# Kernel optimization log

Hardware: AMD Instinct MI355X
Metric: run time of the kernel (lower is better)

The kernel has to match this reference:

```python
import jax, jax.numpy as jnp
import numpy as np

NUM_LAYER = 5
EMB = 300
BN_EPS = 1e-5
NUM_BOND_TYPE = 6
NUM_BOND_DIR = 3
SELF_LOOP_TYPE = 4  # pretrain-gnns self-loop edge attr = [4, 0]


def setup_inputs() -> dict:
    key = jax.random.key(0)
    ks = jax.random.split(key, 12)
    N, E, D = 100000, 250000, EMB
    x = jax.random.normal(ks[0], (N, D), dtype=jnp.float32)
    edge_index = jax.random.randint(ks[1], (2, E), 0, N, dtype=jnp.int64)
    edge_attr = jax.random.randint(ks[2], (E, 2), 0, 3, dtype=jnp.int64)
    L = NUM_LAYER
    W1 = jax.random.normal(ks[3], (L, D, 2 * D), dtype=jnp.float32) * 0.05
    b1 = jnp.zeros((L, 2 * D), dtype=jnp.float32)
    W2 = jax.random.normal(ks[4], (L, 2 * D, D), dtype=jnp.float32) * 0.05
    b2 = jnp.zeros((L, D), dtype=jnp.float32)
    E1 = jax.random.normal(ks[5], (L, NUM_BOND_TYPE, D), dtype=jnp.float32) * 0.05
    E2 = jax.random.normal(ks[6], (L, NUM_BOND_DIR, D), dtype=jnp.float32) * 0.05
    gamma = jnp.ones((L, D), dtype=jnp.float32)
    beta = jnp.zeros((L, D), dtype=jnp.float32)
    return {"x": x, "edge_index": edge_index, "edge_attr": edge_attr,
            "W1": W1, "b1": b1, "W2": W2, "b2": b2,
            "E1": E1, "E2": E2, "gamma": gamma, "beta": beta}


def reference(x, edge_index, edge_attr, W1, b1, W2, b2, E1, E2, gamma, beta):
    N = x.shape[0]
    src, dst = edge_index[0], edge_index[1]
    bt, bd = edge_attr[:, 0], edge_attr[:, 1]
    h = x
    for l in range(NUM_LAYER):
        # GINEConv: message = x_j + edge_embedding, aggr='add', with self loops
        edge_emb = E1[l][bt] + E2[l][bd]                 # [E, D]
        self_emb = E1[l][SELF_LOOP_TYPE] + E2[l][0]      # [D]
        msg = h[src] + edge_emb                          # [E, D] gather
        agg = jax.ops.segment_sum(msg, dst, num_segments=N) + h + self_emb
        # update MLP: Linear(D,2D) -> ReLU -> Linear(2D,D)
        m = jax.nn.relu(agg @ W1[l] + b1[l]) @ W2[l] + b2[l]
        # BatchNorm1d in training mode (batch stats over nodes, biased var)
        mu = m.mean(axis=0)
        var = m.var(axis=0)
        m = (m - mu) * jax.lax.rsqrt(var + BN_EPS) * gamma[l] + beta[l]
        if l < NUM_LAYER - 1:  # ReLU on all but last layer; dropout ratio 0 -> no-op
            m = jax.nn.relu(m)
        h = m
    return h  # JK == 'last'
```

## Files before the change

kernel.cpp:

```cpp
#include <hip/hip_runtime.h>
#include <hip/hip_bf16.h>

#define NN 100000
#define NE 250000
#define DD 300
#define DDB 304
#define NL 5
#define MPAD 100096
#define KA1 320
#define N1 608
#define N1T 640
#define K2 608
#define N2T 384
#define NBLK 391
#define NCMB 19

typedef __attribute__((ext_vector_type(8))) short short8;
typedef __attribute__((ext_vector_type(4))) float f32x4;

#define GLBP(x) ((const __attribute__((address_space(1))) unsigned int*)(x))
#define LDSP(x) ((__attribute__((address_space(3))) unsigned int*)(x))
#define WAITV(N) asm volatile("s_waitcnt vmcnt(" #N ")" ::: "memory")

__device__ __forceinline__ ushort f2bf(float f){
  unsigned u = __float_as_uint(f);
  u += 0x7FFFu + ((u >> 16) & 1u);
  return (ushort)(u >> 16);
}
__device__ __forceinline__ float bf2f(ushort h){
  return __uint_as_float((unsigned)h << 16);
}
__device__ __forceinline__ unsigned pk2(float a, float b){
  return (unsigned)f2bf(a) | ((unsigned)f2bf(b) << 16);
}

__global__ void prep_weights(const float* __restrict__ W1, const float* __restrict__ W2,
                             ushort* __restrict__ W1T, ushort* __restrict__ W2T){
  int idx = blockIdx.x * 256 + threadIdx.x;
  const int total1 = NL * N1T * KA1;
  const int total2 = NL * N2T * K2;
  if (idx < total1){
    int l = idx / (N1T * KA1);
    int rem = idx % (N1T * KA1);
    int n = rem / KA1, k = rem % KA1;
    float v = (n < 2*DD && k < DD) ? W1[(size_t)l*DD*2*DD + (size_t)k*2*DD + n] : 0.0f;
    W1T[idx] = f2bf(v);
  } else {
    int idx2 = idx - total1;
    if (idx2 < total2){
      int l = idx2 / (N2T * K2);
      int rem = idx2 % (N2T * K2);
      int n = rem / K2, k = rem % K2;
      float v = (n < DD && k < 2*DD) ? W2[(size_t)l*2*DD*DD + (size_t)k*DD + n] : 0.0f;
      W2T[idx2] = f2bf(v);
    }
  }
}

__global__ void prep_ctab(const float* __restrict__ E1, const float* __restrict__ E2,
                          float* __restrict__ ctab){
  int idx = blockIdx.x * 256 + threadIdx.x;
  if (idx >= NL * NCMB * DDB) return;
  int l = idx / (NCMB * DDB);
  int rem = idx % (NCMB * DDB);
  int c = rem / DDB, d = rem % DDB;
  float v = 0.0f;
  if (d < DD){
    int bt = (c < 18) ? (c / 3) : 4;
    int bd = (c < 18) ? (c % 3) : 0;
    v = E1[(size_t)l*6*DD + bt*DD + d] + E2[(size_t)l*3*DD + bd*DD + d];
  }
  ctab[idx] = v;
}

__global__ void csr_count(const int* __restrict__ ei, int* __restrict__ deg){
  int e = blockIdx.x * 256 + threadIdx.x;
  if (e < NE) atomicAdd(&deg[ei[NE + e]], 1);
}

__global__ void scan_blk(const int* __restrict__ deg, int* __restrict__ rs, int* __restrict__ bsum){
  __shared__ int tmp[256];
  int i = blockIdx.x * 256 + threadIdx.x;
  int v = (i < NN) ? deg[i] : 0;
  tmp[threadIdx.x] = v;
  __syncthreads();
  #pragma unroll
  for (int off = 1; off < 256; off <<= 1){
    int t = (threadIdx.x >= off) ? tmp[threadIdx.x - off] : 0;
    __syncthreads();
    tmp[threadIdx.x] += t;
    __syncthreads();
  }
  if (i < NN) rs[i] = tmp[threadIdx.x] - v;
  if (threadIdx.x == 255) bsum[blockIdx.x] = tmp[255];
}

__global__ void scan_top(int* __restrict__ bsum){
  __shared__ int tmp[512];
  int v = (threadIdx.x < NBLK) ? bsum[threadIdx.x] : 0;
  tmp[threadIdx.x] = v;
  __syncthreads();
  #pragma unroll
  for (int off = 1; off < 512; off <<= 1){
    int t = (threadIdx.x >= off) ? tmp[threadIdx.x - off] : 0;
    __syncthreads();
    tmp[threadIdx.x] += t;
    __syncthreads();
  }
  if (threadIdx.x < NBLK) bsum[threadIdx.x] = tmp[threadIdx.x] - v;
}

__global__ void scan_add(int* __restrict__ rs, const int* __restrict__ bsum){
  int i = blockIdx.x * 256 + threadIdx.x;
  if (i < NN) rs[i] += bsum[blockIdx.x];
  if (i == 0) rs[NN] = NE;
}

__global__ void csr_fill(const int* __restrict__ ei, const int* __restrict__ ea,
                         const int* __restrict__ rs, int* __restrict__ cursor,
                         int* __restrict__ edges){
  int e = blockIdx.x * 256 + threadIdx.x;
  if (e < NE){
    int dst = ei[NE + e];
    int src = ei[e];
    int c = ea[2*e] * 3 + ea[2*e + 1];
    int p = rs[dst] + atomicAdd(&cursor[dst], 1);
    edges[p] = src | (c << 20);
  }
}

template<int HBF>
__global__ __launch_bounds__(256) void gather_agg(
    const void* __restrict__ hp, const float2* __restrict__ ss,
    const float* __restrict__ ctab_l,
    const int* __restrict__ rs, const int* __restrict__ edges,
    ushort* __restrict__ agg)
{
  int lane = threadIdx.x & 63;
  int wq = __builtin_amdgcn_readfirstlane(threadIdx.x >> 6);
  int wid = blockIdx.x * 4 + wq;
  int nw = gridDim.x * 4;
  int dA = lane * 4;
  int dB = 256 + lane * 4;
  bool laneB  = (lane < 16);
  bool validB = (dB + 3 < DD + 3) && (dB < DD);

  float scA[4], shA[4], scB[4], shB[4];
  if (HBF){
    #pragma unroll
    for (int j = 0; j < 4; ++j){
      float2 s = ss[dA + j]; scA[j] = s.x; shA[j] = s.y;
    }
    if (validB){
      #pragma unroll
      for (int j = 0; j < 4; ++j){
        float2 s = ss[dB + j]; scB[j] = s.x; shB[j] = s.y;
      }
    }
  }

  const float*  hf = (const float*)hp;
  const ushort* hb = (const ushort*)hp;
  const float* ctS = ctab_l + 18*DDB;

  for (int row = wid; row < MPAD; row += nw){
    float a0=0,a1=0,a2=0,a3=0, b0=0,b1=0,b2=0,b3=0;
    if (row < NN){
      {
        if (HBF){
          uint2 hw = *(const uint2*)(hb + (size_t)row*DDB + dA);
          float h0=bf2f((ushort)hw.x), h1=bf2f((ushort)(hw.x>>16));
          float h2=bf2f((ushort)hw.y), h3=bf2f((ushort)(hw.y>>16));
          a0 = fmaxf(h0*scA[0]+shA[0],0.f) + ctS[dA+0];
          a1 = fmaxf(h1*scA[1]+shA[1],0.f) + ctS[dA+1];
          a2 = fmaxf(h2*scA[2]+shA[2],0.f) + ctS[dA+2];
          a3 = fmaxf(h3*scA[3]+shA[3],0.f) + ctS[dA+3];
          if (validB){
            uint2 hv = *(const uint2*)(hb + (size_t)row*DDB + dB);
            b0 = fmaxf(bf2f((ushort)hv.x)*scB[0]+shB[0],0.f)      + ctS[dB+0];
            b1 = fmaxf(bf2f((ushort)(hv.x>>16))*scB[1]+shB[1],0.f)+ ctS[dB+1];
            b2 = fmaxf(bf2f((ushort)hv.y)*scB[2]+shB[2],0.f)      + ctS[dB+2];
            b3 = fmaxf(bf2f((ushort)(hv.y>>16))*scB[3]+shB[3],0.f)+ ctS[dB+3];
          }
        } else {
          float4 hv = *(const float4*)(hf + (size_t)row*DD + dA);
          a0 = hv.x + ctS[dA+0]; a1 = hv.y + ctS[dA+1];
          a2 = hv.z + ctS[dA+2]; a3 = hv.w + ctS[dA+3];
          if (validB){
            float4 hv2 = *(const float4*)(hf + (size_t)row*DD + dB);
            b0 = hv2.x + ctS[dB+0]; b1 = hv2.y + ctS[dB+1];
            b2 = hv2.z + ctS[dB+2]; b3 = hv2.w + ctS[dB+3];
          }
        }
      }
      int p = rs[row], pe = rs[row + 1];
      for (; p < pe; ++p){
        int ew = edges[p];
        int src = ew & 0xFFFFF;
        const float* ct = ctab_l + (ew >> 20)*DDB;
        if (HBF){
          uint2 hw = *(const uint2*)(hb + (size_t)src*DDB + dA);
          float h0=bf2f((ushort)hw.x), h1=bf2f((ushort)(hw.x>>16));
          float h2=bf2f((ushort)hw.y), h3=bf2f((ushort)(hw.y>>16));
          a0 += fmaxf(h0*scA[0]+shA[0],0.f) + ct[dA+0];
          a1 += fmaxf(h1*scA[1]+shA[1],0.f) + ct[dA+1];
          a2 += fmaxf(h2*scA[2]+shA[2],0.f) + ct[dA+2];
          a3 += fmaxf(h3*scA[3]+shA[3],0.f) + ct[dA+3];
          if (validB){
            uint2 hv = *(const uint2*)(hb + (size_t)src*DDB + dB);
            b0 += fmaxf(bf2f((ushort)hv.x)*scB[0]+shB[0],0.f)      + ct[dB+0];
            b1 += fmaxf(bf2f((ushort)(hv.x>>16))*scB[1]+shB[1],0.f)+ ct[dB+1];
            b2 += fmaxf(bf2f((ushort)hv.y)*scB[2]+shB[2],0.f)      + ct[dB+2];
            b3 += fmaxf(bf2f((ushort)(hv.y>>16))*scB[3]+shB[3],0.f)+ ct[dB+3];
          }
        } else {
          float4 hv = *(const float4*)(hf + (size_t)src*DD + dA);
          a0 += hv.x + ct[dA+0]; a1 += hv.y + ct[dA+1];
          a2 += hv.z + ct[dA+2]; a3 += hv.w + ct[dA+3];
          if (validB){
            float4 hv2 = *(const float4*)(hf + (size_t)src*DD + dB);
            b0 += hv2.x + ct[dB+0]; b1 += hv2.y + ct[dB+1];
            b2 += hv2.z + ct[dB+2]; b3 += hv2.w + ct[dB+3];
          }
        }
      }
    }
    ushort* ag = agg + (size_t)row*KA1;
    uint2 oA; oA.x = pk2(a0, a1); oA.y = pk2(a2, a3);
    *(uint2*)(ag + dA) = oA;
    if (laneB){
      uint2 oB;
      if (validB){ oB.x = pk2(b0, b1); oB.y = pk2(b2, b3); }
      else       { oB.x = 0; oB.y = 0; }
      *(uint2*)(ag + dB) = oB;
    }
  }
}

template<int OUT_BF16, int RELU, int STATS>
__global__ __launch_bounds__(512) void gemm_lds(
    const ushort* __restrict__ A, int lda,
    const ushort* __restrict__ B, int ldb,
    void* __restrict__ Cp, int ldc,
    int kTiles, const float* __restrict__ bias, int biasN,
    int Mvalid, int Nvalid, int nColTiles, float* __restrict__ statf)
{
  __shared__ ushort As[3][8192];
  __shared__ ushort Bs[3][4096];
  int tid = threadIdx.x;
  int lane = tid & 63, w = tid >> 6;
  int wm = (w >> 1) * 64, wn = (w & 1) * 64;

  int nwg = gridDim.x;
  int q = nwg >> 3, r = nwg & 7;
  int xcd = blockIdx.x & 7, idx = blockIdx.x >> 3;
  int bid = (xcd < r ? xcd * (q + 1) : r * (q + 1) + (xcd - r) * q) + idx;
  int m0 = (bid / nColTiles) * 256;
  int n0 = (bid % nColTiles) * 128;

  int r0 = tid >> 2;
  int kc = ((tid & 3) ^ ((tid >> 3) & 3)) * 8;
  const ushort* Ap = A + (size_t)(m0 + r0)*lda + kc;
  const ushort* Bp = B + (size_t)(n0 + r0)*ldb + kc;

  f32x4 acc[4][4] = {};

#define STAGE(buf, kt) do { \
    int _ko = (kt) * 32; \
    __builtin_amdgcn_global_load_lds(GLBP(Ap + _ko),                   LDSP(&As[buf][w*512]),        16, 0, 0); \
    __builtin_amdgcn_global_load_lds(GLBP(Ap + _ko + (size_t)128*lda), LDSP(&As[buf][w*512 + 4096]), 16, 0, 0); \
    __builtin_amdgcn_global_load_lds(GLBP(Bp + _ko),                   LDSP(&Bs[buf][w*512]),        16, 0, 0); \
  } while (0)

  STAGE(0, 0);
  STAGE(1, 1);
  WAITV(3);
  __builtin_amdgcn_s_barrier();

  int fr = lane & 15;
  int ko8 = (((lane >> 4) ^ ((fr >> 1) & 3))) * 8;
  int cur = 0;
  for (int kt = 0; kt < kTiles; ++kt){
    int sb = cur + 2; if (sb >= 3) sb -= 3;
    if (kt + 2 < kTiles) STAGE(sb, kt + 2);
    short8 af[4], bfv[4];
    #pragma unroll
    for (int i = 0; i < 4; ++i)
      af[i] = *(const short8*)&As[cur][(wm + i*16 + fr)*32 + ko8];
    #pragma unroll
    for (int j = 0; j < 4; ++j)
      bfv[j] = *(const short8*)&Bs[cur][(wn + j*16 + fr)*32 + ko8];
    #pragma unroll
    for (int i = 0; i < 4; ++i)
      #pragma unroll
      for (int j = 0; j < 4; ++j)
        acc[i][j] = __builtin_amdgcn_mfma_f32_16x16x32_bf16(af[i], bfv[j], acc[i][j], 0, 0, 0);
    if (kt + 1 < kTiles){
      if (kt + 2 < kTiles) WAITV(3);
      else                 WAITV(0);
      __builtin_amdgcn_s_barrier();
    }
    cur = cur + 1; if (cur >= 3) cur = 0;
  }
#undef STAGE

  int cc = lane & 15, cr = (lane >> 4) * 4;
  float ps[4], pq[4];
  if (STATS){
    #pragma unroll
    for (int j = 0; j < 4; ++j){ ps[j] = 0.0f; pq[j] = 0.0f; }
  }
  #pragma unroll
  for (int i = 0; i < 4; ++i){
    #pragma unroll
    for (int j = 0; j < 4; ++j){
      int col = n0 + wn + j*16 + cc;
      if (col >= Nvalid) continue;
      float bv = (col < biasN) ? bias[col] : 0.0f;
      #pragma unroll
      for (int r2 = 0; r2 < 4; ++r2){
        int row = m0 + wm + i*16 + cr + r2;
        if (row < Mvalid){
          float v = acc[i][j][r2] + bv;
          if (RELU) v = fmaxf(v, 0.0f);
          if (OUT_BF16) ((ushort*)Cp)[(size_t)row*ldc + col] = f2bf(v);
          else          ((float*) Cp)[(size_t)row*ldc + col] = v;
          if (STATS){ ps[j] += v; pq[j] += v * v; }
        }
      }
    }
  }
  if (STATS){
    #pragma unroll
    for (int j = 0; j < 4; ++j){
      float s = ps[j], qv = pq[j];
      s += __shfl_xor(s, 16); qv += __shfl_xor(qv, 16);
      s += __shfl_xor(s, 32); qv += __shfl_xor(qv, 32);
      int col = n0 + wn + j*16 + cc;
      if ((lane >> 4) == 0 && col < Nvalid){
        unsafeAtomicAdd(&statf[col], s);
        unsafeAtomicAdd(&statf[N2T + col], qv);
      }
    }
  }
}

__global__ void make_norm(const float* __restrict__ statf, const float* __restrict__ gamma,
                          const float* __restrict__ beta, float2* __restrict__ ss){
  int d = threadIdx.x;
  if (d >= DD) return;
  double mu = (double)statf[d] / (double)NN;
  double var = (double)statf[N2T + d] / (double)NN - mu * mu;
  float inv = rsqrtf((float)var + 1e-5f);
  float sc = inv * gamma[d];
  ss[d] = make_float2(sc, beta[d] - (float)mu * sc);
}

__global__ void apply_norm(const float* __restrict__ m2, const float2* __restrict__ ss,
                           float* __restrict__ out){
  int row = blockIdx.x;
  int d = threadIdx.x;
  if (d >= DD) return;
  float2 s = ss[d];
  out[(size_t)row*DD + d] = m2[(size_t)row*DD + d] * s.x + s.y;
}

extern "C" void kernel_launch(void* const* d_in, const int* in_sizes, int n_in,
                              void* d_out, int out_size, void* d_ws, size_t ws_size,
                              hipStream_t stream) {
  const float* x     = (const float*)d_in[0];
  const int*   ei    = (const int*)  d_in[1];
  const int*   ea    = (const int*)  d_in[2];
  const float* W1    = (const float*)d_in[3];
  const float* b1    = (const float*)d_in[4];
  const float* W2    = (const float*)d_in[5];
  const float* b2    = (const float*)d_in[6];
  const float* E1    = (const float*)d_in[7];
  const float* E2    = (const float*)d_in[8];
  const float* gamma = (const float*)d_in[9];
  const float* beta  = (const float*)d_in[10];

  char* p = (char*)d_ws;
  float*  m2buf = (float*) p; p += (size_t)NN * DD * 4;
  ushort* m2bf  = (ushort*)p; p += (size_t)NN * DDB * 2;
  ushort* agg   = (ushort*)p; p += (size_t)MPAD * KA1 * 2;
  ushort* m1    = (ushort*)p; p += (size_t)MPAD * N1 * 2;
  ushort* W1T   = (ushort*)p; p += (size_t)NL * N1T * KA1 * 2;
  ushort* W2T   = (ushort*)p; p += (size_t)NL * N2T * K2 * 2;
  float*  ctab  = (float*) p; p += (size_t)NL * NCMB * DDB * 4;
  int*    deg   = (int*)   p; p += (size_t)NN * 4;
  int*    rs    = (int*)   p; p += (size_t)(NN + 16) * 4;
  int*    bsum  = (int*)   p; p += (size_t)512 * 4;
  int*    cursor= (int*)   p; p += (size_t)NN * 4;
  int*    edges = (int*)   p; p += (size_t)NE * 4;
  float*  statf = (float*) p; p += (size_t)2 * N2T * 4;
  float2* ss    = (float2*)p;

  {
    int total = NL*N1T*KA1 + NL*N2T*K2;
    prep_weights<<<(total + 255)/256, 256, 0, stream>>>(W1, W2, W1T, W2T);
    int tc = NL * NCMB * DDB;
    prep_ctab<<<(tc + 255)/256, 256, 0, stream>>>(E1, E2, ctab);
  }
  hipMemsetAsync(deg, 0, (size_t)NN*4, stream);
  hipMemsetAsync(cursor, 0, (size_t)NN*4, stream);
  csr_count<<<(NE + 255)/256, 256, 0, stream>>>(ei, deg);
  scan_blk<<<NBLK, 256, 0, stream>>>(deg, rs, bsum);
  scan_top<<<1, 512, 0, stream>>>(bsum);
  scan_add<<<NBLK, 256, 0, stream>>>(rs, bsum);
  csr_fill<<<(NE + 255)/256, 256, 0, stream>>>(ei, ea, rs, cursor, edges);

  for (int l = 0; l < NL; ++l){
    const float* ctab_l = ctab + (size_t)l * NCMB * DDB;

    if (l == 0)
      gather_agg<0><<<1024, 256, 0, stream>>>(x, nullptr, ctab_l, rs, edges, agg);
    else
      gather_agg<1><<<1024, 256, 0, stream>>>(m2bf, ss, ctab_l, rs, edges, agg);

    gemm_lds<1,1,0><<<(MPAD/256) * (N1T/128), 512, 0, stream>>>(
        agg, KA1, W1T + (size_t)l*N1T*KA1, KA1, m1, N1, KA1/32,
        b1 + (size_t)l*2*DD, 2*DD, MPAD, N1, N1T/128, nullptr);

    hipMemsetAsync(statf, 0, (size_t)2*N2T*4, stream);

    if (l < NL - 1)
      gemm_lds<1,0,1><<<(MPAD/256) * (N2T/128), 512, 0, stream>>>(
          m1, N1, W2T + (size_t)l*N2T*K2, K2, m2bf, DDB, K2/32,
          b2 + (size_t)l*DD, DD, NN, DD, N2T/128, statf);
    else
      gemm_lds<0,0,1><<<(MPAD/256) * (N2T/128), 512, 0, stream>>>(
          m1, N1, W2T + (size_t)l*N2T*K2, K2, m2buf, DD, K2/32,
          b2 + (size_t)l*DD, DD, NN, DD, N2T/128, statf);

    make_norm<<<1, 320, 0, stream>>>(statf, gamma + (size_t)l*DD, beta + (size_t)l*DD, ss);
  }
  apply_norm<<<NN, 320, 0, stream>>>(m2buf, ss, (float*)d_out);
}
```

Before: 1.529 ms.

## Shrink GEMM tile to 128x128 with 256 threads and 5-stage LDS pipeline

The GEMM workgroup drops from 512 threads on a 256x128 tile to 256 threads on a 128x128 tile. The LDS pipeline grows from 3 to 5 buffers with a prefetch distance of 4 and matching vmcnt waits. The aim is more workgroups, better occupancy and deeper latency hiding for the short K loops (10 and 19 tiles). The cost is less A-tile reuse per workgroup and more B traffic, plus a cosmetic cleanup of the gather kernel.

```diff
diff --git a/kernel.cpp b/kernel.cpp
--- a/kernel.cpp
+++ b/kernel.cpp
@@ -143,7 +143,7 @@
   int dA = lane * 4;
   int dB = 256 + lane * 4;
   bool laneB  = (lane < 16);
-  bool validB = (dB + 3 < DD + 3) && (dB < DD);
+  bool validB = (dB < DD);
 
   float scA[4], shA[4], scB[4], shB[4];
   if (HBF){
@@ -166,31 +166,27 @@
   for (int row = wid; row < MPAD; row += nw){
     float a0=0,a1=0,a2=0,a3=0, b0=0,b1=0,b2=0,b3=0;
     if (row < NN){
-      {
-        if (HBF){
-          uint2 hw = *(const uint2*)(hb + (size_t)row*DDB + dA);
-          float h0=bf2f((ushort)hw.x), h1=bf2f((ushort)(hw.x>>16));
-          float h2=bf2f((ushort)hw.y), h3=bf2f((ushort)(hw.y>>16));
-          a0 = fmaxf(h0*scA[0]+shA[0],0.f) + ctS[dA+0];
-          a1 = fmaxf(h1*scA[1]+shA[1],0.f) + ctS[dA+1];
-          a2 = fmaxf(h2*scA[2]+shA[2],0.f) + ctS[dA+2];
-          a3 = fmaxf(h3*scA[3]+shA[3],0.f) + ctS[dA+3];
-          if (validB){
-            uint2 hv = *(const uint2*)(hb + (size_t)row*DDB + dB);
-            b0 = fmaxf(bf2f((ushort)hv.x)*scB[0]+shB[0],0.f)      + ctS[dB+0];
-            b1 = fmaxf(bf2f((ushort)(hv.x>>16))*scB[1]+shB[1],0.f)+ ctS[dB+1];
-            b2 = fmaxf(bf2f((ushort)hv.y)*scB[2]+shB[2],0.f)      + ctS[dB+2];
-            b3 = fmaxf(bf2f((ushort)(hv.y>>16))*scB[3]+shB[3],0.f)+ ctS[dB+3];
-          }
-        } else {
-          float4 hv = *(const float4*)(hf + (size_t)row*DD + dA);
-          a0 = hv.x + ctS[dA+0]; a1 = hv.y + ctS[dA+1];
-          a2 = hv.z + ctS[dA+2]; a3 = hv.w + ctS[dA+3];
-          if (validB){
-            float4 hv2 = *(const float4*)(hf + (size_t)row*DD + dB);
-            b0 = hv2.x + ctS[dB+0]; b1 = hv2.y + ctS[dB+1];
-            b2 = hv2.z + ctS[dB+2]; b3 = hv2.w + ctS[dB+3];
-          }
+      if (HBF){
+        uint2 hw = *(const uint2*)(hb + (size_t)row*DDB + dA);
+        a0 = fmaxf(bf2f((ushort)hw.x)*scA[0]+shA[0],0.f)      + ctS[dA+0];
+        a1 = fmaxf(bf2f((ushort)(hw.x>>16))*scA[1]+shA[1],0.f)+ ctS[dA+1];
+        a2 = fmaxf(bf2f((ushort)hw.y)*scA[2]+shA[2],0.f)      + ctS[dA+2];
+        a3 = fmaxf(bf2f((ushort)(hw.y>>16))*scA[3]+shA[3],0.f)+ ctS[dA+3];
+        if (validB){
+          uint2 hv = *(const uint2*)(hb + (size_t)row*DDB + dB);
+          b0 = fmaxf(bf2f((ushort)hv.x)*scB[0]+shB[0],0.f)      + ctS[dB+0];
+          b1 = fmaxf(bf2f((ushort)(hv.x>>16))*scB[1]+shB[1],0.f)+ ctS[dB+1];
+          b2 = fmaxf(bf2f((ushort)hv.y)*scB[2]+shB[2],0.f)      + ctS[dB+2];
+          b3 = fmaxf(bf2f((ushort)(hv.y>>16))*scB[3]+shB[3],0.f)+ ctS[dB+3];
+        }
+      } else {
+        float4 hv = *(const float4*)(hf + (size_t)row*DD + dA);
+        a0 = hv.x + ctS[dA+0]; a1 = hv.y + ctS[dA+1];
+        a2 = hv.z + ctS[dA+2]; a3 = hv.w + ctS[dA+3];
+        if (validB){
+          float4 hv2 = *(const float4*)(hf + (size_t)row*DD + dB);
+          b0 = hv2.x + ctS[dB+0]; b1 = hv2.y + ctS[dB+1];
+          b2 = hv2.z + ctS[dB+2]; b3 = hv2.w + ctS[dB+3];
         }
       }
       int p = rs[row], pe = rs[row + 1];
@@ -200,12 +196,10 @@
         const float* ct = ctab_l + (ew >> 20)*DDB;
         if (HBF){
           uint2 hw = *(const uint2*)(hb + (size_t)src*DDB + dA);
-          float h0=bf2f((ushort)hw.x), h1=bf2f((ushort)(hw.x>>16));
-          float h2=bf2f((ushort)hw.y), h3=bf2f((ushort)(hw.y>>16));
-          a0 += fmaxf(h0*scA[0]+shA[0],0.f) + ct[dA+0];
-          a1 += fmaxf(h1*scA[1]+shA[1],0.f) + ct[dA+1];
-          a2 += fmaxf(h2*scA[2]+shA[2],0.f) + ct[dA+2];
-          a3 += fmaxf(h3*scA[3]+shA[3],0.f) + ct[dA+3];
+          a0 += fmaxf(bf2f((ushort)hw.x)*scA[0]+shA[0],0.f)      + ct[dA+0];
+          a1 += fmaxf(bf2f((ushort)(hw.x>>16))*scA[1]+shA[1],0.f)+ ct[dA+1];
+          a2 += fmaxf(bf2f((ushort)hw.y)*scA[2]+shA[2],0.f)      + ct[dA+2];
+          a3 += fmaxf(bf2f((ushort)(hw.y>>16))*scA[3]+shA[3],0.f)+ ct[dA+3];
           if (validB){
             uint2 hv = *(const uint2*)(hb + (size_t)src*DDB + dB);
             b0 += fmaxf(bf2f((ushort)hv.x)*scB[0]+shB[0],0.f)      + ct[dB+0];
@@ -238,15 +232,15 @@
 }
 
 template<int OUT_BF16, int RELU, int STATS>
-__global__ __launch_bounds__(512) void gemm_lds(
+__global__ __launch_bounds__(256) void gemm_lds(
     const ushort* __restrict__ A, int lda,
     const ushort* __restrict__ B, int ldb,
     void* __restrict__ Cp, int ldc,
     int kTiles, const float* __restrict__ bias, int biasN,
     int Mvalid, int Nvalid, int nColTiles, float* __restrict__ statf)
 {
-  __shared__ ushort As[3][8192];
-  __shared__ ushort Bs[3][4096];
+  __shared__ ushort As[5][4096];
+  __shared__ ushort Bs[5][4096];
   int tid = threadIdx.x;
   int lane = tid & 63, w = tid >> 6;
   int wm = (w >> 1) * 64, wn = (w & 1) * 64;
@@ -255,7 +249,7 @@
   int q = nwg >> 3, r = nwg & 7;
   int xcd = blockIdx.x & 7, idx = blockIdx.x >> 3;
   int bid = (xcd < r ? xcd * (q + 1) : r * (q + 1) + (xcd - r) * q) + idx;
-  int m0 = (bid / nColTiles) * 256;
+  int m0 = (bid / nColTiles) * 128;
   int n0 = (bid % nColTiles) * 128;
 
   int r0 = tid >> 2;
@@ -267,22 +261,22 @@
 
 #define STAGE(buf, kt) do { \
     int _ko = (kt) * 32; \
-    __builtin_amdgcn_global_load_lds(GLBP(Ap + _ko),                   LDSP(&As[buf][w*512]),        16, 0, 0); \
-    __builtin_amdgcn_global_load_lds(GLBP(Ap + _ko + (size_t)128*lda), LDSP(&As[buf][w*512 + 4096]), 16, 0, 0); \
-    __builtin_amdgcn_global_load_lds(GLBP(Bp + _ko),                   LDSP(&Bs[buf][w*512]),        16, 0, 0); \
+    __builtin_amdgcn_global_load_lds(GLBP(Ap + _ko),                  LDSP(&As[buf][w*512]),        16, 0, 0); \
+    __builtin_amdgcn_global_load_lds(GLBP(Ap + _ko + (size_t)64*lda), LDSP(&As[buf][w*512 + 2048]), 16, 0, 0); \
+    __builtin_amdgcn_global_load_lds(GLBP(Bp + _ko),                  LDSP(&Bs[buf][w*512]),        16, 0, 0); \
+    __builtin_amdgcn_global_load_lds(GLBP(Bp + _ko + (size_t)64*ldb), LDSP(&Bs[buf][w*512 + 2048]), 16, 0, 0); \
   } while (0)
 
-  STAGE(0, 0);
-  STAGE(1, 1);
-  WAITV(3);
+  STAGE(0, 0); STAGE(1, 1); STAGE(2, 2); STAGE(3, 3);
+  WAITV(12);
   __builtin_amdgcn_s_barrier();
 
   int fr = lane & 15;
   int ko8 = (((lane >> 4) ^ ((fr >> 1) & 3))) * 8;
   int cur = 0;
   for (int kt = 0; kt < kTiles; ++kt){
-    int sb = cur + 2; if (sb >= 3) sb -= 3;
-    if (kt + 2 < kTiles) STAGE(sb, kt + 2);
+    int sb = cur + 4; if (sb >= 5) sb -= 5;
+    if (kt + 4 < kTiles) STAGE(sb, kt + 4);
     short8 af[4], bfv[4];
     #pragma unroll
     for (int i = 0; i < 4; ++i)
@@ -296,11 +290,14 @@
       for (int j = 0; j < 4; ++j)
         acc[i][j] = __builtin_amdgcn_mfma_f32_16x16x32_bf16(af[i], bfv[j], acc[i][j], 0, 0, 0);
     if (kt + 1 < kTiles){
-      if (kt + 2 < kTiles) WAITV(3);
-      else                 WAITV(0);
+      int rem = kTiles - kt;
+      if      (rem >= 5) WAITV(12);
+      else if (rem == 4) WAITV(8);
+      else if (rem == 3) WAITV(4);
+      else               WAITV(0);
       __builtin_amdgcn_s_barrier();
     }
-    cur = cur + 1; if (cur >= 3) cur = 0;
+    cur = cur + 1; if (cur >= 5) cur = 0;
   }
 #undef STAGE
 
@@ -418,18 +415,18 @@
     else
       gather_agg<1><<<1024, 256, 0, stream>>>(m2bf, ss, ctab_l, rs, edges, agg);
 
-    gemm_lds<1,1,0><<<(MPAD/256) * (N1T/128), 512, 0, stream>>>(
+    gemm_lds<1,1,0><<<(MPAD/128) * (N1T/128), 256, 0, stream>>>(
         agg, KA1, W1T + (size_t)l*N1T*KA1, KA1, m1, N1, KA1/32,
         b1 + (size_t)l*2*DD, 2*DD, MPAD, N1, N1T/128, nullptr);
 
     hipMemsetAsync(statf, 0, (size_t)2*N2T*4, stream);
 
     if (l < NL - 1)
-      gemm_lds<1,0,1><<<(MPAD/256) * (N2T/128), 512, 0, stream>>>(
+      gemm_lds<1,0,1><<<(MPAD/128) * (N2T/128), 256, 0, stream>>>(
           m1, N1, W2T + (size_t)l*N2T*K2, K2, m2bf, DDB, K2/32,
           b2 + (size_t)l*DD, DD, NN, DD, N2T/128, statf);
     else
-      gemm_lds<0,0,1><<<(MPAD/256) * (N2T/128), 512, 0, stream>>>(
+      gemm_lds<0,0,1><<<(MPAD/128) * (N2T/128), 256, 0, stream>>>(
           m1, N1, W2T + (size_t)l*N2T*K2, K2, m2buf, DD, K2/32,
           b2 + (size_t)l*DD, DD, NN, DD, N2T/128, statf);
 
```

Result: slower. 1.888 ms (+23.5%).

## Add persistent first-layer GEMM keeping a weight column tile resident in LDS

Applied to the files above, without the earlier changes.

Replaces the generic tiled GEMM for the first MLP linear with a persistent kernel. Each workgroup loads one 128-column slice of W1 into LDS once, then streams 3-4 row tiles of the aggregated features through a triple-buffered async global-to-LDS pipeline. Bias and ReLU are applied in registers, and the output is staged through LDS so it can be written with coalesced 16-byte stores. This is meant to cut repeated weight loads and per-tile launch overhead, at the cost of much more LDS per block and lower occupancy. The gather kernel gets only cosmetic cleanups.

```diff
diff --git a/kernel.cpp b/kernel.cpp
--- a/kernel.cpp
+++ b/kernel.cpp
@@ -143,7 +143,7 @@
   int dA = lane * 4;
   int dB = 256 + lane * 4;
   bool laneB  = (lane < 16);
-  bool validB = (dB + 3 < DD + 3) && (dB < DD);
+  bool validB = (dB < DD);
 
   float scA[4], shA[4], scB[4], shB[4];
   if (HBF){
@@ -164,33 +164,29 @@
   const float* ctS = ctab_l + 18*DDB;
 
   for (int row = wid; row < MPAD; row += nw){
-    float a0=0,a1=0,a2=0,a3=0, b0=0,b1=0,b2=0,b3=0;
+    float a0=0,a1=0,a2=0,a3=0, b0=0,b1v=0,b2v=0,b3=0;
     if (row < NN){
-      {
-        if (HBF){
-          uint2 hw = *(const uint2*)(hb + (size_t)row*DDB + dA);
-          float h0=bf2f((ushort)hw.x), h1=bf2f((ushort)(hw.x>>16));
-          float h2=bf2f((ushort)hw.y), h3=bf2f((ushort)(hw.y>>16));
-          a0 = fmaxf(h0*scA[0]+shA[0],0.f) + ctS[dA+0];
-          a1 = fmaxf(h1*scA[1]+shA[1],0.f) + ctS[dA+1];
-          a2 = fmaxf(h2*scA[2]+shA[2],0.f) + ctS[dA+2];
-          a3 = fmaxf(h3*scA[3]+shA[3],0.f) + ctS[dA+3];
-          if (validB){
-            uint2 hv = *(const uint2*)(hb + (size_t)row*DDB + dB);
-            b0 = fmaxf(bf2f((ushort)hv.x)*scB[0]+shB[0],0.f)      + ctS[dB+0];
-            b1 = fmaxf(bf2f((ushort)(hv.x>>16))*scB[1]+shB[1],0.f)+ ctS[dB+1];
-            b2 = fmaxf(bf2f((ushort)hv.y)*scB[2]+shB[2],0.f)      + ctS[dB+2];
-            b3 = fmaxf(bf2f((ushort)(hv.y>>16))*scB[3]+shB[3],0.f)+ ctS[dB+3];
-          }
-        } else {
-          float4 hv = *(const float4*)(hf + (size_t)row*DD + dA);
-          a0 = hv.x + ctS[dA+0]; a1 = hv.y + ctS[dA+1];
-          a2 = hv.z + ctS[dA+2]; a3 = hv.w + ctS[dA+3];
-          if (validB){
-            float4 hv2 = *(const float4*)(hf + (size_t)row*DD + dB);
-            b0 = hv2.x + ctS[dB+0]; b1 = hv2.y + ctS[dB+1];
-            b2 = hv2.z + ctS[dB+2]; b3 = hv2.w + ctS[dB+3];
-          }
+      if (HBF){
+        uint2 hw = *(const uint2*)(hb + (size_t)row*DDB + dA);
+        a0 = fmaxf(bf2f((ushort)hw.x)*scA[0]+shA[0],0.f)      + ctS[dA+0];
+        a1 = fmaxf(bf2f((ushort)(hw.x>>16))*scA[1]+shA[1],0.f)+ ctS[dA+1];
+        a2 = fmaxf(bf2f((ushort)hw.y)*scA[2]+shA[2],0.f)      + ctS[dA+2];
+        a3 = fmaxf(bf2f((ushort)(hw.y>>16))*scA[3]+shA[3],0.f)+ ctS[dA+3];
+        if (validB){
+          uint2 hv = *(const uint2*)(hb + (size_t)row*DDB + dB);
+          b0  = fmaxf(bf2f((ushort)hv.x)*scB[0]+shB[0],0.f)      + ctS[dB+0];
+          b1v = fmaxf(bf2f((ushort)(hv.x>>16))*scB[1]+shB[1],0.f)+ ctS[dB+1];
+          b2v = fmaxf(bf2f((ushort)hv.y)*scB[2]+shB[2],0.f)      + ctS[dB+2];
+          b3  = fmaxf(bf2f((ushort)(hv.y>>16))*scB[3]+shB[3],0.f)+ ctS[dB+3];
+        }
+      } else {
+        float4 hv = *(const float4*)(hf + (size_t)row*DD + dA);
+        a0 = hv.x + ctS[dA+0]; a1 = hv.y + ctS[dA+1];
+        a2 = hv.z + ctS[dA+2]; a3 = hv.w + ctS[dA+3];
+        if (validB){
+          float4 hv2 = *(const float4*)(hf + (size_t)row*DD + dB);
+          b0 = hv2.x + ctS[dB+0]; b1v = hv2.y + ctS[dB+1];
+          b2v = hv2.z + ctS[dB+2]; b3 = hv2.w + ctS[dB+3];
         }
       }
       int p = rs[row], pe = rs[row + 1];
@@ -200,18 +196,16 @@
         const float* ct = ctab_l + (ew >> 20)*DDB;
         if (HBF){
           uint2 hw = *(const uint2*)(hb + (size_t)src*DDB + dA);
-          float h0=bf2f((ushort)hw.x), h1=bf2f((ushort)(hw.x>>16));
-          float h2=bf2f((ushort)hw.y), h3=bf2f((ushort)(hw.y>>16));
-          a0 += fmaxf(h0*scA[0]+shA[0],0.f) + ct[dA+0];
-          a1 += fmaxf(h1*scA[1]+shA[1],0.f) + ct[dA+1];
-          a2 += fmaxf(h2*scA[2]+shA[2],0.f) + ct[dA+2];
-          a3 += fmaxf(h3*scA[3]+shA[3],0.f) + ct[dA+3];
+          a0 += fmaxf(bf2f((ushort)hw.x)*scA[0]+shA[0],0.f)      + ct[dA+0];
+          a1 += fmaxf(bf2f((ushort)(hw.x>>16))*scA[1]+shA[1],0.f)+ ct[dA+1];
+          a2 += fmaxf(bf2f((ushort)hw.y)*scA[2]+shA[2],0.f)      + ct[dA+2];
+          a3 += fmaxf(bf2f((ushort)(hw.y>>16))*scA[3]+shA[3],0.f)+ ct[dA+3];
           if (validB){
             uint2 hv = *(const uint2*)(hb + (size_t)src*DDB + dB);
-            b0 += fmaxf(bf2f((ushort)hv.x)*scB[0]+shB[0],0.f)      + ct[dB+0];
-            b1 += fmaxf(bf2f((ushort)(hv.x>>16))*scB[1]+shB[1],0.f)+ ct[dB+1];
-            b2 += fmaxf(bf2f((ushort)hv.y)*scB[2]+shB[2],0.f)      + ct[dB+2];
-            b3 += fmaxf(bf2f((ushort)(hv.y>>16))*scB[3]+shB[3],0.f)+ ct[dB+3];
+            b0  += fmaxf(bf2f((ushort)hv.x)*scB[0]+shB[0],0.f)      + ct[dB+0];
+            b1v += fmaxf(bf2f((ushort)(hv.x>>16))*scB[1]+shB[1],0.f)+ ct[dB+1];
+            b2v += fmaxf(bf2f((ushort)hv.y)*scB[2]+shB[2],0.f)      + ct[dB+2];
+            b3  += fmaxf(bf2f((ushort)(hv.y>>16))*scB[3]+shB[3],0.f)+ ct[dB+3];
           }
         } else {
           float4 hv = *(const float4*)(hf + (size_t)src*DD + dA);
@@ -219,8 +213,8 @@
           a2 += hv.z + ct[dA+2]; a3 += hv.w + ct[dA+3];
           if (validB){
             float4 hv2 = *(const float4*)(hf + (size_t)src*DD + dB);
-            b0 += hv2.x + ct[dB+0]; b1 += hv2.y + ct[dB+1];
-            b2 += hv2.z + ct[dB+2]; b3 += hv2.w + ct[dB+3];
+            b0 += hv2.x + ct[dB+0]; b1v += hv2.y + ct[dB+1];
+            b2v += hv2.z + ct[dB+2]; b3 += hv2.w + ct[dB+3];
           }
         }
       }
@@ -230,15 +224,138 @@
     *(uint2*)(ag + dA) = oA;
     if (laneB){
       uint2 oB;
-      if (validB){ oB.x = pk2(b0, b1); oB.y = pk2(b2, b3); }
+      if (validB){ oB.x = pk2(b0, b1v); oB.y = pk2(b2v, b3); }
       else       { oB.x = 0; oB.y = 0; }
       *(uint2*)(ag + dB) = oB;
     }
   }
 }
 
+__global__ __launch_bounds__(512) void gemm1_persist(
+    const ushort* __restrict__ agg,
+    const ushort* __restrict__ W1T_l,
+    const float* __restrict__ b1_l,
+    ushort* __restrict__ m1)
+{
+  __shared__ ushort Bw[128*KA1];
+  __shared__ ushort As[3][4096];
+  __shared__ ushort Bo[128*144];
+
+  int tid = threadIdx.x;
+  int lane = tid & 63, w = tid >> 6;
+  int wm = (w >> 2) * 64;
+  int wn = (w & 3) * 32;
+
+  int nwg = gridDim.x;
+  int q = nwg >> 3;
+  int xcd = blockIdx.x & 7, bix = blockIdx.x >> 3;
+  int bid = xcd * q + bix;
+  int jcol = bid >> 8;
+  int sub  = bid & 255;
+  int totMT = (sub < 14) ? 4 : 3;
+
+  int fr = lane & 15;
+  int kq = lane >> 4;
+  int ko8 = (kq ^ ((fr >> 1) & 3)) * 8;
+  int cc = fr, cr = kq * 4;
+
+  {
+    const ushort* src = W1T_l + (size_t)jcol * 128 * KA1;
+    #pragma unroll
+    for (int rr = 0; rr < 10; ++rr){
+      int L = rr * 512 + tid;
+      int row = (L * 8) / KA1;
+      int g   = ((L * 8) % KA1) >> 3;
+      uint4 v = *(const uint4*)(src + (size_t)row * KA1 + g * 8);
+      int ph = (g & ~7) | ((g & 7) ^ (row & 7));
+      *(uint4*)&Bw[row * KA1 + ph * 8] = v;
+    }
+  }
+  __syncthreads();
+
+  int r0 = tid >> 2;
+  int kc = ((tid & 3) ^ ((tid >> 3) & 3)) * 8;
+  const ushort* ApS = agg + ((size_t)sub * 128 + r0) * KA1 + kc;
+  int smt = 0, skt = 0, sB = 0;
+#define STAGE1() do { \
+    __builtin_amdgcn_global_load_lds( \
+        GLBP(ApS + (size_t)smt * (256u*128u*KA1) + skt * 32), \
+        LDSP(&As[sB][w*512]), 16, 0, 0); \
+    ++skt; if (skt == 10){ skt = 0; ++smt; } \
+    ++sB; if (sB == 3) sB = 0; \
+  } while (0)
+
+  STAGE1(); STAGE1();
+  WAITV(1);
+  __builtin_amdgcn_s_barrier();
+
+  int totT = totMT * 10;
+  int cur = 0;
+  for (int mt = 0; mt < totMT; ++mt){
+    int m0 = (sub + (mt << 8)) * 128;
+    f32x4 acc[4][2] = {};
+    for (int kt = 0; kt < 10; ++kt){
+      int T = mt * 10 + kt;
+      if (T + 2 < totT) STAGE1();
+      short8 af[4], bw[2];
+      #pragma unroll
+      for (int i = 0; i < 4; ++i)
+        af[i] = *(const short8*)&As[cur][(wm + i*16 + fr)*32 + ko8];
+      int g = kt * 4 + kq;
+      int ph = (g & ~7) | ((g & 7) ^ (fr & 7));
+      #pragma unroll
+      for (int j2 = 0; j2 < 2; ++j2)
+        bw[j2] = *(const short8*)&Bw[(wn + j2*16 + fr)*KA1 + ph*8];
+      #pragma unroll
+      for (int i = 0; i < 4; ++i)
+        #pragma unroll
+        for (int j2 = 0; j2 < 2; ++j2)
+          acc[i][j2] = __builtin_amdgcn_mfma_f32_16x16x32_bf16(af[i], bw[j2], acc[i][j2], 0, 0, 0);
+      if (T + 1 < totT){
+        if (T + 2 < totT) WAITV(1);
+        else              WAITV(0);
+        __builtin_amdgcn_s_barrier();
+      }
+      cur = cur + 1; if (cur == 3) cur = 0;
+    }
+    #pragma unroll
+    for (int i = 0; i < 4; ++i){
+      #pragma unroll
+      for (int j2 = 0; j2 < 2; ++j2){
+        int col = wn + j2*16 + cc;
+        int gcol = jcol*128 + col;
+        float bv = (gcol < 2*DD) ? b1_l[gcol] : 0.0f;
+        #pragma unroll
+        for (int r2 = 0; r2 < 4; ++r2){
+          int row = wm + i*16 + cr + r2;
+          Bo[row*144 + col] = f2bf(fmaxf(acc[i][j2][r2] + bv, 0.0f));
+        }
+      }
+    }
+    asm volatile("s_waitcnt lgkmcnt(0)" ::: "memory");
+    __builtin_amdgcn_sched_barrier(0);
+    __builtin_amdgcn_s_barrier();
+    {
+      int row = tid >> 2, colb = (tid & 3) * 32;
+      const uint4* bo = (const uint4*)&Bo[row*144 + colb];
+      ushort* dst = m1 + (size_t)(m0 + row) * N1 + jcol*128 + colb;
+      #pragma unroll
+      for (int qd = 0; qd < 4; ++qd){
+        int gcol = jcol*128 + colb + qd*8;
+        if (gcol + 8 <= N1){
+          uint4 v = bo[qd];
+          *(uint4*)(dst + qd*8) = v;
+        }
+      }
+    }
+    WAITV(1);
+    __builtin_amdgcn_s_barrier();
+  }
+#undef STAGE1
+}
+
 template<int OUT_BF16, int RELU, int STATS>
-__global__ __launch_bounds__(512) void gemm_lds(
+__global__ __launch_bounds__(512) void gemm_256(
     const ushort* __restrict__ A, int lda,
     const ushort* __restrict__ B, int ldb,
     void* __restrict__ Cp, int ldc,
@@ -418,18 +535,17 @@
     else
       gather_agg<1><<<1024, 256, 0, stream>>>(m2bf, ss, ctab_l, rs, edges, agg);
 
-    gemm_lds<1,1,0><<<(MPAD/256) * (N1T/128), 512, 0, stream>>>(
-        agg, KA1, W1T + (size_t)l*N1T*KA1, KA1, m1, N1, KA1/32,
-        b1 + (size_t)l*2*DD, 2*DD, MPAD, N1, N1T/128, nullptr);
+    gemm1_persist<<<1280, 512, 0, stream>>>(
+        agg, W1T + (size_t)l*N1T*KA1, b1 + (size_t)l*2*DD, m1);
 
     hipMemsetAsync(statf, 0, (size_t)2*N2T*4, stream);
 
     if (l < NL - 1)
-      gemm_lds<1,0,1><<<(MPAD/256) * (N2T/128), 512, 0, stream>>>(
+      gemm_256<1,0,1><<<(MPAD/256) * (N2T/128), 512, 0, stream>>>(
           m1, N1, W2T + (size_t)l*N2T*K2, K2, m2bf, DDB, K2/32,
           b2 + (size_t)l*DD, DD, NN, DD, N2T/128, statf);
     else
-      gemm_lds<0,0,1><<<(MPAD/256) * (N2T/128), 512, 0, stream>>>(
+      gemm_256<0,0,1><<<(MPAD/256) * (N2T/128), 512, 0, stream>>>(
           m1, N1, W2T + (size_t)l*N2T*K2, K2, m2buf, DD, K2/32,
           b2 + (size_t)l*DD, DD, NN, DD, N2T/128, statf);
 
```

Result: slower. 1.714 ms (+12.1%).
